# Kernel tuning notes

Hardware: AMD Instinct MI355X
Metric: run time of the kernel (lower is better)

Reference implementation:

```python
import jax, jax.numpy as jnp
import numpy as np

NUM_HEADS = 8
SEG_LEN = 1024
NUM_SEG = 4
D = 2560
M = 128  # num_memory_tokens


def setup_inputs() -> dict:
    key = jax.random.key(0)
    ks = jax.random.split(key, 16)
    B, S = 2, 4096
    std = 0.02

    def w(k, shape):
        return jax.random.normal(k, shape, dtype=jnp.float32) * std

    return {
        "hidden_states": jax.random.normal(ks[0], (B, S, D), dtype=jnp.float32),
        # memory read params
        "initial_memory": w(ks[1], (1, M, D)),
        "wq_r": w(ks[2], (D, D)),
        "wk_r": w(ks[3], (D, D)),
        "wv_r": w(ks[4], (D, D)),
        "wo_r": w(ks[5], (D, D)),
        "wg_r": w(ks[6], (D, D)),
        "bg_r": jnp.zeros((D,), jnp.float32),
        # memory write params
        "write_queries": w(ks[7], (1, M, D)),
        "wq_w": w(ks[8], (D, D)),
        "wk_w": w(ks[9], (D, D)),
        "wv_w": w(ks[10], (D, D)),
        "wo_w": w(ks[11], (D, D)),
        "wg_w": w(ks[12], (2 * D, D)),
        "bg_w": jnp.zeros((D,), jnp.float32),
    }


def _mha(q, k, v, num_heads):
    """Standard multi-head attention: q (B,Lq,D), k/v (B,Lk,D) -> (B,Lq,D)."""
    B, Lq, d = q.shape
    Lk = k.shape[1]
    hd = d // num_heads
    qh = q.reshape(B, Lq, num_heads, hd)
    kh = k.reshape(B, Lk, num_heads, hd)
    vh = v.reshape(B, Lk, num_heads, hd)
    scores = jnp.einsum('bqhd,bkhd->bhqk', qh, kh) / jnp.sqrt(jnp.asarray(hd, jnp.float32))
    attn = jax.nn.softmax(scores, axis=-1)  # fp32 softmax, as in source
    out = jnp.einsum('bhqk,bkhd->bqhd', attn, vh)
    return out.reshape(B, Lq, d)


def reference(hidden_states, initial_memory, wq_r, wk_r, wv_r, wo_r, wg_r, bg_r,
              write_queries, wq_w, wk_w, wv_w, wo_w, wg_w, bg_w):
    B, S, d = hidden_states.shape
    memory = None
    outs = []
    for i in range(NUM_SEG):  # fixed small segment loop (sequential recurrence)
        seg = hidden_states[:, i * SEG_LEN:(i + 1) * SEG_LEN]
        mem = jnp.broadcast_to(initial_memory, (B, M, d)) if memory is None else memory
        # --- memory read: cross-attention from segment tokens to memory bank ---
        ctx = _mha(seg @ wq_r, mem @ wk_r, mem @ wv_r, NUM_HEADS)
        gate = jax.nn.sigmoid(seg @ wg_r + bg_r)
        h = seg + gate * (ctx @ wo_r)
        # process_fn is identity (DEQ block not part of this module)
        # --- memory write: memory queries attend to processed segment ---
        mq = jnp.broadcast_to(write_queries, (B, M, d))
        new_mem = _mha(mq @ wq_w, h @ wk_w, h @ wv_w, NUM_HEADS) @ wo_w
        if memory is None:
            memory = new_mem
        else:
            g = jax.nn.sigmoid(jnp.concatenate([memory, new_mem], axis=-1) @ wg_w + bg_w)
            memory = g * new_mem + (1.0 - g) * memory
        outs.append(h)
    return jnp.concatenate(outs, axis=1)
```

## Files before the change

kernel.cpp:

```cpp
#include <hip/hip_runtime.h>
#include <hip/hip_bf16.h>
#include <math.h>

#define BB 2
#define SS 4096
#define DDIM 2560
#define MMEM 128
#define NH 8
#define HDIM 320
#define SEG 1024
#define NSEG 4

typedef unsigned short u16;
typedef __attribute__((ext_vector_type(8))) short short8;
typedef __attribute__((ext_vector_type(4))) float f32x4;

__device__ __forceinline__ u16 f2b(float x) {
  __hip_bfloat16 h = __float2bfloat16(x);
  return *reinterpret_cast<u16*>(&h);
}

__device__ __forceinline__ void gll16(const u16* g, u16* l) {
  __builtin_amdgcn_global_load_lds(
      (__attribute__((address_space(1))) void*)g,
      (__attribute__((address_space(3))) void*)l, 16, 0, 0);
}

struct OutDesc {
  float* f; u16* b; u16* bt; const float* bias;
  long ld; long ldt; long s1; long s2;
};

__global__ __launch_bounds__(256) void gemm_bt(
    const u16* __restrict__ A, const u16* __restrict__ Bt,
    OutDesc o0, OutDesc o1, int Nsplit,
    int N, int K, long lda, long ldb,
    long sA1, long sA2, long sB1, long sB2,
    int Z1, float alpha)
{
  __shared__ __align__(16) u16 sm[8192];
  u16* As = sm;
  u16* Bs = sm + 4096;

  int z = blockIdx.z;
  int z1 = z % Z1, z2 = z / Z1;
  const u16* Az = A + (long)z1 * sA1 + (long)z2 * sA2 + (long)blockIdx.x * 128 * lda;
  const u16* Bz = Bt + (long)z1 * sB1 + (long)z2 * sB2;

  int tN = blockIdx.y * 128;
  int t = threadIdx.x;
  int lane = t & 63, w = t >> 6;
  int wm = w & 1, wn = w >> 1;

  int rr = t >> 2;
  int c8 = (t & 3) << 3;
  int n0 = tN + rr;      if (n0 > N - 1) n0 = N - 1;
  int n1 = tN + 64 + rr; if (n1 > N - 1) n1 = N - 1;
  const u16* ga0 = Az + (long)rr * lda + c8;
  const u16* ga1 = Az + (long)(rr + 64) * lda + c8;
  const u16* gb0 = Bz + (long)n0 * ldb + c8;
  const u16* gb1 = Bz + (long)n1 * ldb + c8;
  u16* lA0 = As + t * 8;
  u16* lA1 = As + 2048 + t * 8;
  u16* lB0 = Bs + t * 8;
  u16* lB1 = Bs + 2048 + t * 8;

  f32x4 acc[4][4];
#pragma unroll
  for (int i = 0; i < 4; i++)
#pragma unroll
    for (int j = 0; j < 4; j++) acc[i][j] = (f32x4){0.f, 0.f, 0.f, 0.f};

  int arow = lane & 15;
  int kq = (lane >> 4) << 3;

  for (int k0 = 0; k0 < K; k0 += 32) {
    gll16(ga0, lA0); gll16(ga1, lA1);
    gll16(gb0, lB0); gll16(gb1, lB1);
    ga0 += 32; ga1 += 32; gb0 += 32; gb1 += 32;
    __syncthreads();

    short8 af[4], bfr[4];
#pragma unroll
    for (int i = 0; i < 4; i++)
      af[i] = *(const short8*)(As + (wm * 64 + i * 16 + arow) * 32 + kq);
#pragma unroll
    for (int j = 0; j < 4; j++)
      bfr[j] = *(const short8*)(Bs + (wn * 64 + j * 16 + arow) * 32 + kq);
#pragma unroll
    for (int i = 0; i < 4; i++)
#pragma unroll
      for (int j = 0; j < 4; j++)
        acc[i][j] = __builtin_amdgcn_mfma_f32_16x16x32_bf16(af[i], bfr[j], acc[i][j], 0, 0, 0);
    __syncthreads();
  }

  int rowb = blockIdx.x * 128 + wm * 64 + ((lane >> 4) << 2);
#pragma unroll
  for (int i = 0; i < 4; i++) {
    int row = rowb + i * 16;
#pragma unroll
    for (int j = 0; j < 4; j++) {
      int cl = tN + wn * 64 + j * 16 + arow;
      if (cl >= N) continue;
      const OutDesc& d = (cl < Nsplit) ? o0 : o1;
      int c = (cl < Nsplit) ? cl : cl - Nsplit;
      long co = (long)z1 * d.s1 + (long)z2 * d.s2;
      float bv = d.bias ? d.bias[c] : 0.f;
      float x0 = acc[i][j][0] * alpha + bv;
      float x1 = acc[i][j][1] * alpha + bv;
      float x2 = acc[i][j][2] * alpha + bv;
      float x3 = acc[i][j][3] * alpha + bv;
      if (d.f) {
        d.f[co + (long)(row + 0) * d.ld + c] = x0;
        d.f[co + (long)(row + 1) * d.ld + c] = x1;
        d.f[co + (long)(row + 2) * d.ld + c] = x2;
        d.f[co + (long)(row + 3) * d.ld + c] = x3;
      }
      if (d.b) {
        d.b[co + (long)(row + 0) * d.ld + c] = f2b(x0);
        d.b[co + (long)(row + 1) * d.ld + c] = f2b(x1);
        d.b[co + (long)(row + 2) * d.ld + c] = f2b(x2);
        d.b[co + (long)(row + 3) * d.ld + c] = f2b(x3);
      }
      if (d.bt) {
        ushort4 v;
        v.x = f2b(x0); v.y = f2b(x1); v.z = f2b(x2); v.w = f2b(x3);
        *(ushort4*)(d.bt + co + (long)c * d.ldt + row) = v;
      }
    }
  }
}

__global__ __launch_bounds__(256) void gemm_bt_sk(
    const u16* __restrict__ A, const u16* __restrict__ Bt,
    float* __restrict__ C, long cs,
    int N, int K, int Kc, int SK,
    long lda, long ldb, long sA1, long sA2, long sB1, long sB2,
    int Z1, float alpha)
{
  __shared__ __align__(16) u16 sm[8192];
  u16* As = sm;
  u16* Bs = sm + 4096;

  int zz = blockIdx.z;
  int ks = zz % SK;
  int z  = zz / SK;
  int z1 = z % Z1, z2 = z / Z1;
  const u16* Az = A + (long)z1 * sA1 + (long)z2 * sA2 + (long)blockIdx.x * 128 * lda;
  const u16* Bz = Bt + (long)z1 * sB1 + (long)z2 * sB2;

  int tN = blockIdx.y * 128;
  int t = threadIdx.x;
  int lane = t & 63, w = t >> 6;
  int wm = w & 1, wn = w >> 1;

  int rr = t >> 2;
  int c8 = (t & 3) << 3;
  int n0 = tN + rr;      if (n0 > N - 1) n0 = N - 1;
  int n1 = tN + 64 + rr; if (n1 > N - 1) n1 = N - 1;
  int kb = ks * Kc;
  int ke = kb + Kc; if (ke > K) ke = K;
  const u16* ga0 = Az + (long)rr * lda + kb + c8;
  const u16* ga1 = Az + (long)(rr + 64) * lda + kb + c8;
  const u16* gb0 = Bz + (long)n0 * ldb + kb + c8;
  const u16* gb1 = Bz + (long)n1 * ldb + kb + c8;
  u16* lA0 = As + t * 8;
  u16* lA1 = As + 2048 + t * 8;
  u16* lB0 = Bs + t * 8;
  u16* lB1 = Bs + 2048 + t * 8;

  f32x4 acc[4][4];
#pragma unroll
  for (int i = 0; i < 4; i++)
#pragma unroll
    for (int j = 0; j < 4; j++) acc[i][j] = (f32x4){0.f, 0.f, 0.f, 0.f};

  int arow = lane & 15;
  int kq = (lane >> 4) << 3;

  for (int k0 = kb; k0 < ke; k0 += 32) {
    gll16(ga0, lA0); gll16(ga1, lA1);
    gll16(gb0, lB0); gll16(gb1, lB1);
    ga0 += 32; ga1 += 32; gb0 += 32; gb1 += 32;
    __syncthreads();

    short8 af[4], bfr[4];
#pragma unroll
    for (int i = 0; i < 4; i++)
      af[i] = *(const short8*)(As + (wm * 64 + i * 16 + arow) * 32 + kq);
#pragma unroll
    for (int j = 0; j < 4; j++)
      bfr[j] = *(const short8*)(Bs + (wn * 64 + j * 16 + arow) * 32 + kq);
#pragma unroll
    for (int i = 0; i < 4; i++)
#pragma unroll
      for (int j = 0; j < 4; j++)
        acc[i][j] = __builtin_amdgcn_mfma_f32_16x16x32_bf16(af[i], bfr[j], acc[i][j], 0, 0, 0);
    __syncthreads();
  }

  int rowb = blockIdx.x * 128 + wm * 64 + ((lane >> 4) << 2);
  long zoff = (long)z * cs;
#pragma unroll
  for (int i = 0; i < 4; i++) {
    int row = rowb + i * 16;
#pragma unroll
    for (int j = 0; j < 4; j++) {
      int cl = tN + wn * 64 + j * 16 + arow;
      if (cl >= N) continue;
      float* cp = C + zoff + (long)row * N + cl;
      atomicAdd(cp,            acc[i][j][0] * alpha);
      atomicAdd(cp + N,        acc[i][j][1] * alpha);
      atomicAdd(cp + 2L * N,   acc[i][j][2] * alpha);
      atomicAdd(cp + 3L * N,   acc[i][j][3] * alpha);
    }
  }
}

__global__ void conv_bf16(const float* __restrict__ X, u16* __restrict__ Y, long n4) {
  long i = (long)blockIdx.x * 256 + threadIdx.x;
  if (i < n4) {
    float4 v = ((const float4*)X)[i];
    ushort4 o;
    o.x = f2b(v.x); o.y = f2b(v.y); o.z = f2b(v.z); o.w = f2b(v.w);
    ((ushort4*)Y)[i] = o;
  }
}

__global__ __launch_bounds__(256) void transpose_conv(const float* __restrict__ W, u16* __restrict__ Wt, int K, int N) {
  __shared__ float tile[32][33];
  int nb = blockIdx.x * 32;
  int kb = blockIdx.y * 32;
  int tx = threadIdx.x & 31, ty = threadIdx.x >> 5;
  for (int r = ty; r < 32; r += 8) {
    int k = kb + r, n = nb + tx;
    tile[r][tx] = (k < K && n < N) ? W[(long)k * N + n] : 0.f;
  }
  __syncthreads();
  for (int r = ty; r < 32; r += 8) {
    int n = nb + r, k = kb + tx;
    if (n < N && k < K) Wt[(long)n * K + k] = f2b(tile[tx][r]);
  }
}

__global__ void init_mem(const float* __restrict__ im, float* __restrict__ mf, u16* __restrict__ mb,
                         long perB, long total) {
  long i = (long)blockIdx.x * 256 + threadIdx.x;
  if (i < total) { float v = im[i % perB]; mf[i] = v; mb[i] = f2b(v); }
}

__global__ __launch_bounds__(256) void softmax_rows(const float* __restrict__ S, u16* __restrict__ P, int len) {
  __shared__ float e[1024];
  __shared__ float red[4];
  long row = blockIdx.x;
  const float* x = S + row * (long)len;
  u16* pp = P + row * (long)len;
  int t = threadIdx.x;
  float mx = -3.4e38f;
  for (int i = t; i < len; i += 256) mx = fmaxf(mx, x[i]);
  for (int o = 32; o; o >>= 1) mx = fmaxf(mx, __shfl_xor(mx, o));
  if ((t & 63) == 0) red[t >> 6] = mx;
  __syncthreads();
  mx = fmaxf(fmaxf(red[0], red[1]), fmaxf(red[2], red[3]));
  __syncthreads();
  float sum = 0.f;
  for (int i = t; i < len; i += 256) { float v = __expf(x[i] - mx); e[i] = v; sum += v; }
  for (int o = 32; o; o >>= 1) sum += __shfl_xor(sum, o);
  if ((t & 63) == 0) red[t >> 6] = sum;
  __syncthreads();
  sum = red[0] + red[1] + red[2] + red[3];
  float inv = 1.f / sum;
  for (int i = t; i < len; i += 256) pp[i] = f2b(e[i] * inv);
}

__global__ void h_kernel(const float* __restrict__ hs, const float* __restrict__ gpre,
                         const float* __restrict__ o, float* __restrict__ out,
                         u16* __restrict__ hb, long segoff) {
  long idx = (long)blockIdx.x * 256 + threadIdx.x;
  const long per = (long)SEG * DDIM;
  long b = idx / per, r = idx - b * per;
  long io = b * (long)SS * DDIM + segoff + r;
  float g = 1.f / (1.f + __expf(-gpre[idx]));
  float h = hs[io] + g * o[idx];
  out[io] = h;
  hb[idx] = f2b(h);
}

__global__ void concat_mem(const u16* __restrict__ a, const u16* __restrict__ b, u16* __restrict__ c) {
  long idx = (long)blockIdx.x * 256 + threadIdx.x;
  long row = idx / (2 * DDIM);
  long col = idx - row * (2 * DDIM);
  c[idx] = (col < DDIM) ? a[row * DDIM + col] : b[row * DDIM + col - DDIM];
}

__global__ void update_mem(const float* __restrict__ gp, const float* __restrict__ bias,
                           const float* __restrict__ nm,
                           float* __restrict__ mf, u16* __restrict__ mb) {
  long idx = (long)blockIdx.x * 256 + threadIdx.x;
  int col = (int)(idx % DDIM);
  float g = 1.f / (1.f + __expf(-(gp[idx] + bias[col])));
  float v = g * nm[idx] + (1.f - g) * mf[idx];
  mf[idx] = v;
  mb[idx] = f2b(v);
}


__global__ __launch_bounds__(256) void fin_krv(const float* __restrict__ S,
                                               u16* __restrict__ kr, u16* __restrict__ vt) {
  __shared__ float tile[32][33];
  int cb = blockIdx.x * 32;
  int rb = blockIdx.y * 32;
  int tx = threadIdx.x & 31, ty = threadIdx.x >> 5;
  for (int r = ty; r < 32; r += 8) {
    float v = S[(long)(rb + r) * (2 * DDIM) + cb + tx];
    tile[r][tx] = v;
    if (cb + tx < DDIM) kr[(long)(rb + r) * DDIM + cb + tx] = f2b(v);
  }
  __syncthreads();
  if (cb >= DDIM) {
    for (int r = ty; r < 32; r += 8) {
      int col = cb + r - DDIM;
      vt[(long)col * (BB * MMEM) + rb + tx] = f2b(tile[tx][r]);
    }
  }
}

__global__ void fin_attw(const float* __restrict__ S, u16* __restrict__ att) {
  long idx = (long)blockIdx.x * 256 + threadIdx.x;
  int col = (int)(idx % HDIM);
  long r = idx / HDIM;
  int row = (int)(r % MMEM);
  int z = (int)(r / MMEM);
  int h = z % NH, b = z / NH;
  att[(long)b * MMEM * DDIM + (long)row * DDIM + (long)h * HDIM + col] = f2b(S[idx]);
}

__global__ void fin_nm(const float* __restrict__ S, float* __restrict__ f, u16* __restrict__ b) {
  long idx = (long)blockIdx.x * 256 + threadIdx.x;
  float v = S[idx];
  f[idx] = v;
  b[idx] = f2b(v);
}

__global__ void fin_b16(const float* __restrict__ S, u16* __restrict__ b) {
  long idx = (long)blockIdx.x * 256 + threadIdx.x;
  b[idx] = f2b(S[idx]);
}

static inline OutDesc OD0() {
  OutDesc d; d.f = nullptr; d.b = nullptr; d.bt = nullptr; d.bias = nullptr;
  d.ld = 0; d.ldt = 0; d.s1 = 0; d.s2 = 0; return d;
}

static inline void launch_gemm(hipStream_t st, const void* A, const void* Bt,
    OutDesc o0, OutDesc o1, int Nsplit, int Mr, int N, int K,
    long lda, long ldb, long sA1, long sA2, long sB1, long sB2,
    int Z1, int Z2, float alpha)
{
  dim3 grid(Mr / 128, (N + 127) / 128, Z1 * Z2);
  gemm_bt<<<grid, dim3(256), 0, st>>>((const u16*)A, (const u16*)Bt, o0, o1,
      Nsplit, N, K, lda, ldb, sA1, sA2, sB1, sB2, Z1, alpha);
}

static inline void launch_gemm_sk(hipStream_t st, const void* A, const void* Bt,
    float* C, long cs, int Mr, int N, int K, int SK,
    long lda, long ldb, long sA1, long sA2, long sB1, long sB2,
    int Z1, int Z2, float alpha)
{
  dim3 grid(Mr / 128, (N + 127) / 128, Z1 * Z2 * SK);
  gemm_bt_sk<<<grid, dim3(256), 0, st>>>((const u16*)A, (const u16*)Bt, C, cs,
      N, K, K / SK, SK, lda, ldb, sA1, sA2, sB1, sB2, Z1, alpha);
}

extern "C" void kernel_launch(void* const* d_in, const int* in_sizes, int n_in,
                              void* d_out, int out_size, void* d_ws, size_t ws_size,
                              hipStream_t stream) {
  const float* hs   = (const float*)d_in[0];
  const float* imem = (const float*)d_in[1];
  const float* wq_r = (const float*)d_in[2];
  const float* wk_r = (const float*)d_in[3];
  const float* wv_r = (const float*)d_in[4];
  const float* wo_r = (const float*)d_in[5];
  const float* wg_r = (const float*)d_in[6];
  const float* bg_r = (const float*)d_in[7];
  const float* wqin = (const float*)d_in[8];
  const float* wq_w = (const float*)d_in[9];
  const float* wk_w = (const float*)d_in[10];
  const float* wv_w = (const float*)d_in[11];
  const float* wo_w = (const float*)d_in[12];
  const float* wg_w = (const float*)d_in[13];
  const float* bg_w = (const float*)d_in[14];
  float* out = (float*)d_out;

  const long D = DDIM, M = MMEM, S = SS, B = BB, H = NH, HD = HDIM, L = SEG;
  const float iscale = 1.f / sqrtf((float)HDIM);

  char* p = (char*)d_ws;
  auto alc = [&](size_t bytes) -> void* {
    void* r = (void*)p; p += (bytes + 255) & ~(size_t)255; return r;
  };

  u16* hs_b  = (u16*)alc(B * S * D * 2);
  u16* wqgT  = (u16*)alc(2 * D * D * 2);
  u16* wkvrT = (u16*)alc(2 * D * D * 2);
  u16* wkvwT = (u16*)alc(2 * D * D * 2);
  u16* worT  = (u16*)alc(D * D * 2);
  u16* wowT  = (u16*)alc(D * D * 2);
  u16* wqwT  = (u16*)alc(D * D * 2);
  u16* wgwT  = (u16*)alc(2 * D * D * 2);
  u16* wq_b  = (u16*)alc(M * D * 2);
  u16* q_w   = (u16*)alc(M * D * 2);
  float* mem_f = (float*)alc(B * M * D * 4);
  u16*   mem_b = (u16*)alc(B * M * D * 2);
  float* nm_f  = (float*)alc(B * M * D * 4);
  u16*   nm_b  = (u16*)alc(B * M * D * 2);
  u16* q_r   = (u16*)alc(B * L * D * 2);
  u16* k_r   = (u16*)alc(B * M * D * 2);
  u16* v_rT  = (u16*)alc(D * B * M * 2);
  float* sc_r = (float*)alc(B * H * L * M * 4);
  u16*   pr_r = (u16*)alc(B * H * L * M * 2);
  u16* ctx   = (u16*)alc(B * L * D * 2);
  float* gpre = (float*)alc(B * L * D * 4);
  float* obuf = (float*)alc(B * L * D * 4);
  u16* h_b   = (u16*)alc(B * L * D * 2);
  u16* k_w   = (u16*)alc(B * L * D * 2);
  u16* v_wT  = (u16*)alc(D * B * L * 2);
  float* sc_w = (float*)alc(B * H * M * L * 4);
  u16*   pr_w = (u16*)alc(B * H * M * L * 2);
  u16* att_w = (u16*)alc(B * M * D * 2);
  u16* cat   = (u16*)alc(B * M * 2 * D * 2);
  float* skbuf = (float*)alc((size_t)(B * M) * 2 * D * 4);

  conv_bf16<<<(unsigned)((B * S * D / 4 + 255) / 256), 256, 0, stream>>>(hs, hs_b, B * S * D / 4);
  dim3 tg(D / 32, D / 32);
  transpose_conv<<<tg, 256, 0, stream>>>(wq_r, wqgT,          (int)D, (int)D);
  transpose_conv<<<tg, 256, 0, stream>>>(wg_r, wqgT + D * D,  (int)D, (int)D);
  transpose_conv<<<tg, 256, 0, stream>>>(wk_r, wkvrT,         (int)D, (int)D);
  transpose_conv<<<tg, 256, 0, stream>>>(wv_r, wkvrT + D * D, (int)D, (int)D);
  transpose_conv<<<tg, 256, 0, stream>>>(wk_w, wkvwT,         (int)D, (int)D);
  transpose_conv<<<tg, 256, 0, stream>>>(wv_w, wkvwT + D * D, (int)D, (int)D);
  transpose_conv<<<tg, 256, 0, stream>>>(wo_r, worT, (int)D, (int)D);
  transpose_conv<<<tg, 256, 0, stream>>>(wo_w, wowT, (int)D, (int)D);
  transpose_conv<<<tg, 256, 0, stream>>>(wq_w, wqwT, (int)D, (int)D);
  transpose_conv<<<dim3(D / 32, 2 * D / 32), 256, 0, stream>>>(wg_w, wgwT, (int)(2 * D), (int)D);
  conv_bf16<<<(unsigned)((M * D / 4 + 255) / 256), 256, 0, stream>>>(wqin, wq_b, M * D / 4);
  init_mem<<<(unsigned)((B * M * D + 255) / 256), 256, 0, stream>>>(imem, mem_f, mem_b, M * D, B * M * D);

  {
    hipMemsetAsync(skbuf, 0, (size_t)M * D * 4, stream);
    launch_gemm_sk(stream, wq_b, wqwT, skbuf, 0, (int)M, (int)D, (int)D, 8,
                   D, D, 0, 0, 0, 0, 1, 1, 1.f);
    fin_b16<<<(unsigned)(M * D / 256), 256, 0, stream>>>(skbuf, q_w);
  }

  for (int i = 0; i < NSEG; i++) {
    long so = (long)i * L * D;

    {
      OutDesc o0 = OD0(); o0.b = q_r;  o0.ld = D; o0.s2 = L * D;
      OutDesc o1 = OD0(); o1.f = gpre; o1.ld = D; o1.s2 = L * D; o1.bias = bg_r;
      launch_gemm(stream, hs_b + so, wqgT, o0, o1, (int)D, (int)L, (int)(2 * D), (int)D,
                  D, D, 0, S * D, 0, 0, 1, (int)B, 1.f);
    }
    {
      hipMemsetAsync(skbuf, 0, (size_t)(B * M) * 2 * D * 4, stream);
      launch_gemm_sk(stream, mem_b, wkvrT, skbuf, 0, (int)(B * M), (int)(2 * D), (int)D, 8,
                     D, D, 0, 0, 0, 0, 1, 1, 1.f);
      fin_krv<<<dim3((unsigned)(2 * D / 32), (unsigned)(B * M / 32)), 256, 0, stream>>>(skbuf, k_r, v_rT);
    }
    {
      OutDesc o0 = OD0(); o0.f = sc_r; o0.ld = M; o0.s1 = L * M; o0.s2 = H * L * M;
      launch_gemm(stream, q_r, k_r, o0, OD0(), (int)M, (int)L, (int)M, (int)HD,
                  D, D, HD, L * D, HD, M * D, (int)H, (int)B, iscale);
    }
    softmax_rows<<<(unsigned)(B * H * L), 256, 0, stream>>>(sc_r, pr_r, (int)M);
    {
      OutDesc o0 = OD0(); o0.b = ctx; o0.ld = D; o0.s1 = HD; o0.s2 = L * D;
      launch_gemm(stream, pr_r, v_rT, o0, OD0(), (int)HD, (int)L, (int)HD, (int)M,
                  M, B * M, L * M, H * L * M, HD * B * M, M, (int)H, (int)B, 1.f);
    }
    {
      OutDesc o0 = OD0(); o0.f = obuf; o0.ld = D; o0.s2 = L * D;
      launch_gemm(stream, ctx, worT, o0, OD0(), (int)D, (int)L, (int)D, (int)D,
                  D, D, 0, L * D, 0, 0, 1, (int)B, 1.f);
    }
    h_kernel<<<(unsigned)(B * L * D / 256), 256, 0, stream>>>(hs, gpre, obuf, out, h_b, so);

    {
      OutDesc o0 = OD0(); o0.b = k_w;  o0.ld = D;
      OutDesc o1 = OD0(); o1.bt = v_wT; o1.ldt = B * L;
      launch_gemm(stream, h_b, wkvwT, o0, o1, (int)D, (int)(B * L), (int)(2 * D), (int)D,
                  D, D, 0, 0, 0, 0, 1, 1, 1.f);
    }
    {
      OutDesc o0 = OD0(); o0.f = sc_w; o0.ld = L; o0.s1 = M * L; o0.s2 = H * M * L;
      launch_gemm(stream, q_w, k_w, o0, OD0(), (int)L, (int)M, (int)L, (int)HD,
                  D, D, HD, 0, HD, L * D, (int)H, (int)B, iscale);
    }
    softmax_rows<<<(unsigned)(B * H * M), 256, 0, stream>>>(sc_w, pr_w, (int)L);
    {
      hipMemsetAsync(skbuf, 0, (size_t)B * H * M * HD * 4, stream);
      launch_gemm_sk(stream, pr_w, v_wT, skbuf, (long)M * HD, (int)M, (int)HD, (int)L, 4,
                     L, B * L, M * L, H * M * L, HD * B * L, L, (int)H, (int)B, 1.f);
      fin_attw<<<(unsigned)(B * H * M * HD / 256), 256, 0, stream>>>(skbuf, att_w);
    }
    float* nmf = (i == 0) ? mem_f : nm_f;
    u16*   nmb = (i == 0) ? mem_b : nm_b;
    {
      hipMemsetAsync(skbuf, 0, (size_t)B * M * D * 4, stream);
      launch_gemm_sk(stream, att_w, wowT, skbuf, 0, (int)(B * M), (int)D, (int)D, 8,
                     D, D, 0, 0, 0, 0, 1, 1, 1.f);
      fin_nm<<<(unsigned)(B * M * D / 256), 256, 0, stream>>>(skbuf, nmf, nmb);
    }
    if (i > 0) {
      concat_mem<<<(unsigned)(B * M * 2 * D / 256), 256, 0, stream>>>(mem_b, nm_b, cat);
      hipMemsetAsync(skbuf, 0, (size_t)B * M * D * 4, stream);
      launch_gemm_sk(stream, cat, wgwT, skbuf, 0, (int)(B * M), (int)D, (int)(2 * D), 16,
                     2 * D, 2 * D, 0, 0, 0, 0, 1, 1, 1.f);
      update_mem<<<(unsigned)(B * M * D / 256), 256, 0, stream>>>(skbuf, bg_w, nm_f, mem_f, mem_b);
    }
  }
}
```

Baseline: 2.551 ms.

## Double-buffer GEMM LDS tiles, hoist Q/gate projection out of segment loop

Both GEMM kernels now use two LDS buffers, so the global-to-LDS load of the next K-tile is issued before computing the current one, with one barrier per iteration instead of two. The Q and gate projection over all segments is hoisted into a single large GEMM before the recurrence, since it depends only on the input. The gate pre-activation is stored as bf16 instead of fp32, and the per-segment scratch buffers are aliased onto the no-longer-needed hs_b buffer and onto each other. This aims to hide load latency, cut launch count, raise GEMM occupancy and reduce memory traffic, at the cost of double the LDS per block, slightly lower gate precision, and careful buffer-lifetime reasoning.

```diff
diff --git a/kernel.cpp b/kernel.cpp
--- a/kernel.cpp
+++ b/kernel.cpp
@@ -20,6 +20,13 @@
   return *reinterpret_cast<u16*>(&h);
 }
 
+__device__ __forceinline__ float b2f(u16 v) {
+  unsigned int u = ((unsigned int)v) << 16;
+  float f;
+  __builtin_memcpy(&f, &u, 4);
+  return f;
+}
+
 __device__ __forceinline__ void gll16(const u16* g, u16* l) {
   __builtin_amdgcn_global_load_lds(
       (__attribute__((address_space(1))) void*)g,
@@ -38,9 +45,7 @@
     long sA1, long sA2, long sB1, long sB2,
     int Z1, float alpha)
 {
-  __shared__ __align__(16) u16 sm[8192];
-  u16* As = sm;
-  u16* Bs = sm + 4096;
+  __shared__ __align__(16) u16 sm[16384];
 
   int z = blockIdx.z;
   int z1 = z % Z1, z2 = z / Z1;
@@ -60,10 +65,6 @@
   const u16* ga1 = Az + (long)(rr + 64) * lda + c8;
   const u16* gb0 = Bz + (long)n0 * ldb + c8;
   const u16* gb1 = Bz + (long)n1 * ldb + c8;
-  u16* lA0 = As + t * 8;
-  u16* lA1 = As + 2048 + t * 8;
-  u16* lB0 = Bs + t * 8;
-  u16* lB1 = Bs + 2048 + t * 8;
 
   f32x4 acc[4][4];
 #pragma unroll
@@ -74,12 +75,16 @@
   int arow = lane & 15;
   int kq = (lane >> 4) << 3;
 
-  for (int k0 = 0; k0 < K; k0 += 32) {
-    gll16(ga0, lA0); gll16(ga1, lA1);
-    gll16(gb0, lB0); gll16(gb1, lB1);
+  auto stage = [&](u16* bb) {
+    gll16(ga0, bb + t * 8);
+    gll16(ga1, bb + 2048 + t * 8);
+    gll16(gb0, bb + 4096 + t * 8);
+    gll16(gb1, bb + 6144 + t * 8);
     ga0 += 32; ga1 += 32; gb0 += 32; gb1 += 32;
-    __syncthreads();
-
+  };
+  auto compute = [&](const u16* bb) {
+    const u16* As = bb;
+    const u16* Bs = bb + 4096;
     short8 af[4], bfr[4];
 #pragma unroll
     for (int i = 0; i < 4; i++)
@@ -92,8 +97,21 @@
 #pragma unroll
       for (int j = 0; j < 4; j++)
         acc[i][j] = __builtin_amdgcn_mfma_f32_16x16x32_bf16(af[i], bfr[j], acc[i][j], 0, 0, 0);
+  };
+
+  u16* b0 = sm;
+  u16* b1 = sm + 8192;
+  int nk = K / 32;
+  stage(b0);
+  __syncthreads();
+  for (int it = 1; it < nk; ++it) {
+    u16* sb = (it & 1) ? b1 : b0;
+    u16* cb = (it & 1) ? b0 : b1;
+    stage(sb);
+    compute(cb);
     __syncthreads();
   }
+  compute(((nk - 1) & 1) ? b1 : b0);
 
   int rowb = blockIdx.x * 128 + wm * 64 + ((lane >> 4) << 2);
 #pragma unroll
@@ -139,9 +157,7 @@
     long lda, long ldb, long sA1, long sA2, long sB1, long sB2,
     int Z1, float alpha)
 {
-  __shared__ __align__(16) u16 sm[8192];
-  u16* As = sm;
-  u16* Bs = sm + 4096;
+  __shared__ __align__(16) u16 sm[16384];
 
   int zz = blockIdx.z;
   int ks = zz % SK;
@@ -165,10 +181,6 @@
   const u16* ga1 = Az + (long)(rr + 64) * lda + kb + c8;
   const u16* gb0 = Bz + (long)n0 * ldb + kb + c8;
   const u16* gb1 = Bz + (long)n1 * ldb + kb + c8;
-  u16* lA0 = As + t * 8;
-  u16* lA1 = As + 2048 + t * 8;
-  u16* lB0 = Bs + t * 8;
-  u16* lB1 = Bs + 2048 + t * 8;
 
   f32x4 acc[4][4];
 #pragma unroll
@@ -179,12 +191,16 @@
   int arow = lane & 15;
   int kq = (lane >> 4) << 3;
 
-  for (int k0 = kb; k0 < ke; k0 += 32) {
-    gll16(ga0, lA0); gll16(ga1, lA1);
-    gll16(gb0, lB0); gll16(gb1, lB1);
+  auto stage = [&](u16* bb) {
+    gll16(ga0, bb + t * 8);
+    gll16(ga1, bb + 2048 + t * 8);
+    gll16(gb0, bb + 4096 + t * 8);
+    gll16(gb1, bb + 6144 + t * 8);
     ga0 += 32; ga1 += 32; gb0 += 32; gb1 += 32;
-    __syncthreads();
-
+  };
+  auto compute = [&](const u16* bb) {
+    const u16* As = bb;
+    const u16* Bs = bb + 4096;
     short8 af[4], bfr[4];
 #pragma unroll
     for (int i = 0; i < 4; i++)
@@ -197,8 +213,21 @@
 #pragma unroll
       for (int j = 0; j < 4; j++)
         acc[i][j] = __builtin_amdgcn_mfma_f32_16x16x32_bf16(af[i], bfr[j], acc[i][j], 0, 0, 0);
+  };
+
+  u16* b0 = sm;
+  u16* b1 = sm + 8192;
+  int nk = (ke - kb) / 32;
+  stage(b0);
+  __syncthreads();
+  for (int it = 1; it < nk; ++it) {
+    u16* sb = (it & 1) ? b1 : b0;
+    u16* cb = (it & 1) ? b0 : b1;
+    stage(sb);
+    compute(cb);
     __syncthreads();
   }
+  compute(((nk - 1) & 1) ? b1 : b0);
 
   int rowb = blockIdx.x * 128 + wm * 64 + ((lane >> 4) << 2);
   long zoff = (long)z * cs;
@@ -274,14 +303,14 @@
   for (int i = t; i < len; i += 256) pp[i] = f2b(e[i] * inv);
 }
 
-__global__ void h_kernel(const float* __restrict__ hs, const float* __restrict__ gpre,
+__global__ void h_kernel(const float* __restrict__ hs, const u16* __restrict__ gpre_b,
                          const float* __restrict__ o, float* __restrict__ out,
                          u16* __restrict__ hb, long segoff) {
   long idx = (long)blockIdx.x * 256 + threadIdx.x;
   const long per = (long)SEG * DDIM;
   long b = idx / per, r = idx - b * per;
   long io = b * (long)SS * DDIM + segoff + r;
-  float g = 1.f / (1.f + __expf(-gpre[idx]));
+  float g = 1.f / (1.f + __expf(-b2f(gpre_b[io])));
   float h = hs[io] + g * o[idx];
   out[io] = h;
   hb[idx] = f2b(h);
@@ -402,6 +431,10 @@
   };
 
   u16* hs_b  = (u16*)alc(B * S * D * 2);
+  float* scr  = (float*)hs_b;
+  u16*  ctxkw = (u16*)((char*)hs_b + 20971520);
+  u16*  prvw  = (u16*)((char*)hs_b + 31457280);
+
   u16* wqgT  = (u16*)alc(2 * D * D * 2);
   u16* wkvrT = (u16*)alc(2 * D * D * 2);
   u16* wkvwT = (u16*)alc(2 * D * D * 2);
@@ -415,19 +448,11 @@
   u16*   mem_b = (u16*)alc(B * M * D * 2);
   float* nm_f  = (float*)alc(B * M * D * 4);
   u16*   nm_b  = (u16*)alc(B * M * D * 2);
-  u16* q_r   = (u16*)alc(B * L * D * 2);
+  u16* q_r    = (u16*)alc(B * S * D * 2);
+  u16* gpre_b = (u16*)alc(B * S * D * 2);
   u16* k_r   = (u16*)alc(B * M * D * 2);
   u16* v_rT  = (u16*)alc(D * B * M * 2);
-  float* sc_r = (float*)alc(B * H * L * M * 4);
-  u16*   pr_r = (u16*)alc(B * H * L * M * 2);
-  u16* ctx   = (u16*)alc(B * L * D * 2);
-  float* gpre = (float*)alc(B * L * D * 4);
-  float* obuf = (float*)alc(B * L * D * 4);
-  u16* h_b   = (u16*)alc(B * L * D * 2);
-  u16* k_w   = (u16*)alc(B * L * D * 2);
-  u16* v_wT  = (u16*)alc(D * B * L * 2);
-  float* sc_w = (float*)alc(B * H * M * L * 4);
-  u16*   pr_w = (u16*)alc(B * H * M * L * 2);
+  u16* hbpw  = (u16*)alc(B * L * D * 2);
   u16* att_w = (u16*)alc(B * M * D * 2);
   u16* cat   = (u16*)alc(B * M * 2 * D * 2);
   float* skbuf = (float*)alc((size_t)(B * M) * 2 * D * 4);
@@ -454,15 +479,16 @@
     fin_b16<<<(unsigned)(M * D / 256), 256, 0, stream>>>(skbuf, q_w);
   }
 
+  {
+    OutDesc o0 = OD0(); o0.b = q_r;    o0.ld = D;
+    OutDesc o1 = OD0(); o1.b = gpre_b; o1.ld = D; o1.bias = bg_r;
+    launch_gemm(stream, hs_b, wqgT, o0, o1, (int)D, (int)(B * S), (int)(2 * D), (int)D,
+                D, D, 0, 0, 0, 0, 1, 1, 1.f);
+  }
+
   for (int i = 0; i < NSEG; i++) {
     long so = (long)i * L * D;
 
-    {
-      OutDesc o0 = OD0(); o0.b = q_r;  o0.ld = D; o0.s2 = L * D;
-      OutDesc o1 = OD0(); o1.f = gpre; o1.ld = D; o1.s2 = L * D; o1.bias = bg_r;
-      launch_gemm(stream, hs_b + so, wqgT, o0, o1, (int)D, (int)L, (int)(2 * D), (int)D,
-                  D, D, 0, S * D, 0, 0, 1, (int)B, 1.f);
-    }
     {
       hipMemsetAsync(skbuf, 0, (size_t)(B * M) * 2 * D * 4, stream);
       launch_gemm_sk(stream, mem_b, wkvrT, skbuf, 0, (int)(B * M), (int)(2 * D), (int)D, 8,
@@ -470,38 +496,38 @@
       fin_krv<<<dim3((unsigned)(2 * D / 32), (unsigned)(B * M / 32)), 256, 0, stream>>>(skbuf, k_r, v_rT);
     }
     {
-      OutDesc o0 = OD0(); o0.f = sc_r; o0.ld = M; o0.s1 = L * M; o0.s2 = H * L * M;
-      launch_gemm(stream, q_r, k_r, o0, OD0(), (int)M, (int)L, (int)M, (int)HD,
-                  D, D, HD, L * D, HD, M * D, (int)H, (int)B, iscale);
-    }
-    softmax_rows<<<(unsigned)(B * H * L), 256, 0, stream>>>(sc_r, pr_r, (int)M);
-    {
-      OutDesc o0 = OD0(); o0.b = ctx; o0.ld = D; o0.s1 = HD; o0.s2 = L * D;
-      launch_gemm(stream, pr_r, v_rT, o0, OD0(), (int)HD, (int)L, (int)HD, (int)M,
+      OutDesc o0 = OD0(); o0.f = scr; o0.ld = M; o0.s1 = L * M; o0.s2 = H * L * M;
+      launch_gemm(stream, q_r + so, k_r, o0, OD0(), (int)M, (int)L, (int)M, (int)HD,
+                  D, D, HD, S * D, HD, M * D, (int)H, (int)B, iscale);
+    }
+    softmax_rows<<<(unsigned)(B * H * L), 256, 0, stream>>>(scr, prvw, (int)M);
+    {
+      OutDesc o0 = OD0(); o0.b = ctxkw; o0.ld = D; o0.s1 = HD; o0.s2 = L * D;
+      launch_gemm(stream, prvw, v_rT, o0, OD0(), (int)HD, (int)L, (int)HD, (int)M,
                   M, B * M, L * M, H * L * M, HD * B * M, M, (int)H, (int)B, 1.f);
     }
     {
-      OutDesc o0 = OD0(); o0.f = obuf; o0.ld = D; o0.s2 = L * D;
-      launch_gemm(stream, ctx, worT, o0, OD0(), (int)D, (int)L, (int)D, (int)D,
+      OutDesc o0 = OD0(); o0.f = scr; o0.ld = D; o0.s2 = L * D;
+      launch_gemm(stream, ctxkw, worT, o0, OD0(), (int)D, (int)L, (int)D, (int)D,
                   D, D, 0, L * D, 0, 0, 1, (int)B, 1.f);
     }
-    h_kernel<<<(unsigned)(B * L * D / 256), 256, 0, stream>>>(hs, gpre, obuf, out, h_b, so);
-
-    {
-      OutDesc o0 = OD0(); o0.b = k_w;  o0.ld = D;
-      OutDesc o1 = OD0(); o1.bt = v_wT; o1.ldt = B * L;
-      launch_gemm(stream, h_b, wkvwT, o0, o1, (int)D, (int)(B * L), (int)(2 * D), (int)D,
+    h_kernel<<<(unsigned)(B * L * D / 256), 256, 0, stream>>>(hs, gpre_b, scr, out, hbpw, so);
+
+    {
+      OutDesc o0 = OD0(); o0.b = ctxkw;  o0.ld = D;
+      OutDesc o1 = OD0(); o1.bt = prvw; o1.ldt = B * L;
+      launch_gemm(stream, hbpw, wkvwT, o0, o1, (int)D, (int)(B * L), (int)(2 * D), (int)D,
                   D, D, 0, 0, 0, 0, 1, 1, 1.f);
     }
     {
-      OutDesc o0 = OD0(); o0.f = sc_w; o0.ld = L; o0.s1 = M * L; o0.s2 = H * M * L;
-      launch_gemm(stream, q_w, k_w, o0, OD0(), (int)L, (int)M, (int)L, (int)HD,
+      OutDesc o0 = OD0(); o0.f = scr; o0.ld = L; o0.s1 = M * L; o0.s2 = H * M * L;
+      launch_gemm(stream, q_w, ctxkw, o0, OD0(), (int)L, (int)M, (int)L, (int)HD,
                   D, D, HD, 0, HD, L * D, (int)H, (int)B, iscale);
     }
-    softmax_rows<<<(unsigned)(B * H * M), 256, 0, stream>>>(sc_w, pr_w, (int)L);
+    softmax_rows<<<(unsigned)(B * H * M), 256, 0, stream>>>(scr, hbpw, (int)L);
     {
       hipMemsetAsync(skbuf, 0, (size_t)B * H * M * HD * 4, stream);
-      launch_gemm_sk(stream, pr_w, v_wT, skbuf, (long)M * HD, (int)M, (int)HD, (int)L, 4,
+      launch_gemm_sk(stream, hbpw, prvw, skbuf, (long)M * HD, (int)M, (int)HD, (int)L, 4,
                      L, B * L, M * L, H * M * L, HD * B * L, L, (int)H, (int)B, 1.f);
       fin_attw<<<(unsigned)(B * H * M * HD / 256), 256, 0, stream>>>(skbuf, att_w);
     }
```

New measurement: 2.345 ms. 8.1% less time.
